# Kernel tuning notes

Measured on AMD Instinct MI355X. Metric: run time of the kernel, lower is better.

Reference implementation:

```python
import jax, jax.numpy as jnp
import numpy as np

B, L, F_DIM, H = 4, 384, 640, 128
K_COULOMB = 332.0
DIELECTRIC = 80.0
BN_EPS = 1e-5

# amino-acid charge table, index order 'ACDEFGHIKLMNPQRSTVWY'
_AA = 'ACDEFGHIKLMNPQRSTVWY'
_CHG = {'D': -1.0, 'E': -1.0, 'K': 1.0, 'R': 1.0, 'H': 0.1}
_TABLE = np.zeros((20, 3), dtype=np.float32)
for _i, _aa in enumerate(_AA):
    c = _CHG.get(_aa, 0.0)
    _TABLE[_i, 0 if c > 0 else (1 if c < 0 else 2)] = 1.0
CHG_TABLE = jnp.asarray(_TABLE)


def _conv1d(x, w, b, pad):
    # x: [N, Cin, L], w: [Cout, Cin, K]
    y = jax.lax.conv_general_dilated(x, w, (1,), [(pad, pad)],
                                     dimension_numbers=('NCH', 'OIH', 'NCH'))
    return y + b[None, :, None]


def setup_inputs() -> dict:
    key = jax.random.key(0)
    ks = jax.random.split(key, 32)
    s = 0.05

    def rn(k, shape):
        return (jax.random.normal(k, shape) * s).astype(jnp.float32)

    inp = {
        'features': jax.random.normal(ks[0], (B, L, F_DIM), dtype=jnp.float32),
        'seq_ids': jax.random.randint(ks[1], (B, L), 0, 20, dtype=jnp.int32),
        'structures': (jax.random.normal(ks[2], (B, L, 3)) * 10.0).astype(jnp.float32),
        # charge predictor: Linear(F,H) -> ReLU -> BN(H) -> Linear(H,H//2) -> ReLU -> Linear(H//2,3) -> Softmax
        'W1': rn(ks[3], (F_DIM, H)), 'b1': jnp.zeros((H,), jnp.float32),
        'gamma': jnp.ones((H,), jnp.float32), 'beta': jnp.zeros((H,), jnp.float32),
        'rmean': jnp.zeros((H,), jnp.float32), 'rvar': jnp.ones((H,), jnp.float32),
        'W2': rn(ks[4], (H, H // 2)), 'b2': jnp.zeros((H // 2,), jnp.float32),
        'W3': rn(ks[5], (H // 2, 3)), 'b3': jnp.zeros((3,), jnp.float32),
        # salt bridge detector: Linear(2F+1,H) -> ReLU -> Linear(H,64) -> ReLU -> Linear(64,1) -> Sigmoid
        'sW1': rn(ks[6], (2 * F_DIM + 1, H)), 'sb1': jnp.zeros((H,), jnp.float32),
        'sW2': rn(ks[7], (H, 64)), 'sb2': jnp.zeros((64,), jnp.float32),
        'sW3': rn(ks[8], (64, 1)), 'sb3': jnp.zeros((1,), jnp.float32),
        # potential calculator convs (OIH layout)
        'c1w': rn(ks[9], (16, 1, 5)), 'c1b': jnp.zeros((16,), jnp.float32),
        'c2w': rn(ks[10], (8, 16, 3)), 'c2b': jnp.zeros((8,), jnp.float32),
        'c3w': rn(ks[11], (1, 8, 3)), 'c3b': jnp.zeros((1,), jnp.float32),
    }
    return inp


def reference(features, seq_ids, structures,
              W1, b1, gamma, beta, rmean, rvar, W2, b2, W3, b3,
              sW1, sb1, sW2, sb2, sW3, sb3,
              c1w, c1b, c2w, c2b, c3w, c3b):
    b_, l_, f_ = features.shape

    # true charges from sequence (one-hot pos/neg/neutral)
    true_charges = CHG_TABLE[seq_ids]                               # [B,L,3]

    # --- charge predictor (BatchNorm in eval mode: running stats) ---
    x = features.reshape(-1, f_)
    h = jax.nn.relu(x @ W1 + b1)
    h = gamma * (h - rmean) / jnp.sqrt(rvar + BN_EPS) + beta
    h = jax.nn.relu(h @ W2 + b2)
    pc = jax.nn.softmax(h @ W3 + b3, axis=-1).reshape(b_, l_, 3)    # [B,L,3]

    net_charge = pc[:, :, 0:1] - pc[:, :, 1:2]                      # [B,L,1]

    # --- electrostatic potential: 1D conv stack on [B,1,L] ---
    p = net_charge.transpose(0, 2, 1)                               # [B,1,L]
    p = jax.nn.relu(_conv1d(p, c1w, c1b, 2))
    p = jax.nn.relu(_conv1d(p, c2w, c2b, 1))
    p = _conv1d(p, c3w, c3b, 1)
    potential = p.transpose(0, 2, 1)                                # [B,L,1]

    # --- pairwise distances ---
    diff = structures[:, :, None, :] - structures[:, None, :, :]    # [B,L,L,3]
    D = jnp.sqrt(jnp.sum(diff * diff, axis=-1) + 1e-12)             # [B,L,L]

    # --- salt bridges: vectorized edge-MLP over all (pos i, neg j) pairs ---
    pos = pc[:, :, 0] > pc[:, :, 2]                                 # [B,L]
    neg = pc[:, :, 1] > pc[:, :, 2]                                 # [B,L]
    a, bb, d = sW1[:f_], sW1[f_:2 * f_], sW1[2 * f_]                # split cat([fi,fj,dist]) @ sW1
    fi = features @ a                                               # [B,L,H]
    fj = features @ bb                                              # [B,L,H]
    hid = jax.nn.relu(fi[:, :, None, :] + fj[:, None, :, :] + D[..., None] * d + sb1)  # [B,L,L,H]
    hid2 = jax.nn.relu(hid @ sW2 + sb2)                             # [B,L,L,64]
    prob = jax.nn.sigmoid((hid2 @ sW3 + sb3)[..., 0])               # [B,L,L]
    q = pos[:, :, None] & neg[:, None, :] & (D < 4.0) & (prob > 0.5)
    salt_bridge_masks = (q | q.transpose(0, 2, 1)).astype(jnp.float32)  # [B,L,L]

    # --- Coulomb energy with distance-dependent dielectric ---
    # dielectric = eps * D / 4 -> e_ij = k * q_i q_j / (eps/4 * D^2)
    qc = pc[:, :, 0] - pc[:, :, 1]                                  # [B,L]
    valid = (D < 15.0) & (D > 0.0)
    triu = jnp.triu(jnp.ones((l_, l_), bool), k=1)[None]
    D_safe = jnp.where(valid, D, 1.0)
    e_ij = K_COULOMB * qc[:, :, None] * qc[:, None, :] / ((DIELECTRIC / 4.0) * D_safe * D_safe)
    energy = jnp.sum(jnp.where(valid & triu, e_ij, 0.0), axis=(1, 2))  # [B]

    return (pc, true_charges, net_charge, potential, salt_bridge_masks, energy)
```

## Files before the change

kernel.cpp:

```cpp
#include <hip/hip_runtime.h>

#define LSEQ 384
#define NROWS 1536
#define FDIM 640
#define HDIM 128
#define PART 196608

#define WS_H1P 0
#define WS_FIP (4*PART)
#define WS_FJP (8*PART)
#define WS_FI  (12*PART)
#define WS_FJ  (13*PART)
#define WS_QC  (14*PART)
#define WS_FLAG (WS_QC + NROWS)

#define OUT_PC    0
#define OUT_TC    4608
#define OUT_NET   9216
#define OUT_POT   10752
#define OUT_MASK  12288
#define OUT_EN    602112

typedef float f4 __attribute__((ext_vector_type(4)));

__device__ __forceinline__ void gl16(const float* g, float* l) {
    __builtin_amdgcn_global_load_lds((const __attribute__((address_space(1))) float*)g,
                                     (__attribute__((address_space(3))) float*)l, 16, 0, 0);
}

__global__ __launch_bounds__(256) void k_gemm(const float* __restrict__ X,
                                              const float* __restrict__ W1,
                                              const float* __restrict__ sW1,
                                              float* __restrict__ ws,
                                              float* __restrict__ out) {
    __shared__ __align__(16) float As[2][32][36];
    __shared__ __align__(16) float Bs[2][32][128];

    const int t = threadIdx.x;
    if (blockIdx.x == 0 && blockIdx.y == 0 && t < 4)
        out[OUT_EN + t] = 0.0f;

    const int m0 = blockIdx.x * 32;
    const int by = blockIdx.y;
    const int mat = by >> 2, kz = by & 3;
    const float* W = (mat == 0) ? W1 : (mat == 1 ? sW1 : sW1 + FDIM * HDIM);
    float* O = ws + (mat == 0 ? WS_H1P : (mat == 1 ? WS_FIP : WS_FJP)) + kz * PART;
    const int k0 = kz * 160;

    const int lane = t & 63, wv = t >> 6;
    const int rg = t >> 5;
    const int cg = t & 31;
    const int ar = t >> 3, ac4 = (t & 7) * 4;

    auto stage_B = [&](int buf, int kk) {
        const float* src = W + (long)kk * HDIM;
        float* dst = &Bs[buf][0][0];
#pragma unroll
        for (int i = 0; i < 4; i++) {
            const int c = wv * 4 + i;
            gl16(src + c * 256 + lane * 4, dst + c * 256);
        }
    };

    f4 acc[4];
    acc[0] = acc[1] = acc[2] = acc[3] = (f4){0.f, 0.f, 0.f, 0.f};

    stage_B(0, k0);
    {
        f4 av = *(const f4*)&X[(long)(m0 + ar) * FDIM + k0 + ac4];
        As[0][ac4 + 0][ar] = av[0];
        As[0][ac4 + 1][ar] = av[1];
        As[0][ac4 + 2][ar] = av[2];
        As[0][ac4 + 3][ar] = av[3];
    }
    __syncthreads();

    for (int kt = 0; kt < 5; kt++) {
        const int buf = kt & 1;
        f4 av;
        if (kt < 4) {
            const int kk = k0 + (kt + 1) * 32;
            stage_B(buf ^ 1, kk);
            av = *(const f4*)&X[(long)(m0 + ar) * FDIM + kk + ac4];
        }
        const float* Ab = &As[buf][0][0];
        const float* Bb = &Bs[buf][0][0];
#pragma unroll
        for (int k = 0; k < 32; k++) {
            f4 a = *(const f4*)&Ab[k * 36 + rg * 4];
            f4 b = *(const f4*)&Bb[k * 128 + cg * 4];
            acc[0] += a[0] * b;
            acc[1] += a[1] * b;
            acc[2] += a[2] * b;
            acc[3] += a[3] * b;
        }
        if (kt < 4) {
            As[(buf ^ 1)][ac4 + 0][ar] = av[0];
            As[(buf ^ 1)][ac4 + 1][ar] = av[1];
            As[(buf ^ 1)][ac4 + 2][ar] = av[2];
            As[(buf ^ 1)][ac4 + 3][ar] = av[3];
        }
        __syncthreads();
    }

#pragma unroll
    for (int r = 0; r < 4; r++)
        *(f4*)&O[(long)(m0 + rg * 4 + r) * HDIM + cg * 4] = acc[r];
}

__global__ __launch_bounds__(256) void k_row(float* __restrict__ ws,
                                             const float* __restrict__ b1,
                                             const float* __restrict__ gam,
                                             const float* __restrict__ bet,
                                             const float* __restrict__ rmean,
                                             const float* __restrict__ rvar,
                                             const float* __restrict__ W2,
                                             const float* __restrict__ b2,
                                             const float* __restrict__ W3,
                                             const float* __restrict__ b3,
                                             const int* __restrict__ seq,
                                             float* __restrict__ out) {
    const int t = threadIdx.x, w = t >> 6, lane = t & 63;
    const int row = blockIdx.x * 4 + w;
    const long base = (long)row * 128;
    const float* h1p = ws + WS_H1P;
    const float* fip = ws + WS_FIP;
    const float* fjp = ws + WS_FJP;

    {
        float fi0 = fip[base + lane] + fip[PART + base + lane]
                  + fip[2 * PART + base + lane] + fip[3 * PART + base + lane];
        float fi1 = fip[base + 64 + lane] + fip[PART + base + 64 + lane]
                  + fip[2 * PART + base + 64 + lane] + fip[3 * PART + base + 64 + lane];
        float fj0 = fjp[base + lane] + fjp[PART + base + lane]
                  + fjp[2 * PART + base + lane] + fjp[3 * PART + base + lane];
        float fj1 = fjp[base + 64 + lane] + fjp[PART + base + 64 + lane]
                  + fjp[2 * PART + base + 64 + lane] + fjp[3 * PART + base + 64 + lane];
        ws[WS_FI + base + lane]      = fi0;
        ws[WS_FI + base + 64 + lane] = fi1;
        ws[WS_FJ + base + lane]      = fj0;
        ws[WS_FJ + base + 64 + lane] = fj1;
    }

    float h0 = h1p[base + lane] + h1p[PART + base + lane]
             + h1p[2 * PART + base + lane] + h1p[3 * PART + base + lane];
    float h1 = h1p[base + 64 + lane] + h1p[PART + base + 64 + lane]
             + h1p[2 * PART + base + 64 + lane] + h1p[3 * PART + base + 64 + lane];
    h0 = fmaxf(h0 + b1[lane], 0.0f);
    h1 = fmaxf(h1 + b1[64 + lane], 0.0f);
    h0 = gam[lane]      * (h0 - rmean[lane])      / sqrtf(rvar[lane] + 1e-5f)      + bet[lane];
    h1 = gam[64 + lane] * (h1 - rmean[64 + lane]) / sqrtf(rvar[64 + lane] + 1e-5f) + bet[64 + lane];

    float acc = b2[lane];
#pragma unroll
    for (int cc = 0; cc < 64; cc++) {
        float wv0 = W2[cc * 64 + lane];
        float wv1 = W2[(cc + 64) * 64 + lane];
        float hv0 = __uint_as_float(__builtin_amdgcn_readlane(__float_as_uint(h0), cc));
        float hv1 = __uint_as_float(__builtin_amdgcn_readlane(__float_as_uint(h1), cc));
        acc = fmaf(hv0, wv0, acc);
        acc = fmaf(hv1, wv1, acc);
    }
    float h2 = fmaxf(acc, 0.0f);
    float x0 = h2 * W3[lane * 3 + 0];
    float x1 = h2 * W3[lane * 3 + 1];
    float x2 = h2 * W3[lane * 3 + 2];
#pragma unroll
    for (int o = 32; o > 0; o >>= 1) {
        x0 += __shfl_xor(x0, o, 64);
        x1 += __shfl_xor(x1, o, 64);
        x2 += __shfl_xor(x2, o, 64);
    }
    if (lane == 0) {
        float l0 = x0 + b3[0], l1 = x1 + b3[1], l2 = x2 + b3[2];
        float m = fmaxf(l0, fmaxf(l1, l2));
        float e0 = expf(l0 - m), e1 = expf(l1 - m), e2 = expf(l2 - m);
        float s = e0 + e1 + e2;
        float pc0 = e0 / s, pc1 = e1 / s, pc2 = e2 / s;
        out[OUT_PC + row * 3 + 0] = pc0;
        out[OUT_PC + row * 3 + 1] = pc1;
        out[OUT_PC + row * 3 + 2] = pc2;
        float net = pc0 - pc1;
        out[OUT_NET + row] = net;
        ws[WS_QC + row] = net;
        ((int*)(ws + WS_FLAG))[row] = (pc0 > pc2 ? 1 : 0) | (pc1 > pc2 ? 2 : 0);
        int sid = seq[row];
        float c0 = (sid == 6 || sid == 8 || sid == 14) ? 1.0f : 0.0f;
        float c1 = (sid == 2 || sid == 3) ? 1.0f : 0.0f;
        out[OUT_TC + row * 3 + 0] = c0;
        out[OUT_TC + row * 3 + 1] = c1;
        out[OUT_TC + row * 3 + 2] = (c0 == 0.0f && c1 == 0.0f) ? 1.0f : 0.0f;
    }
}

__device__ __forceinline__ float mlp_eval(const float* __restrict__ fi, const float* __restrict__ fj,
                                          int gi, int gj, float D,
                                          float dv0, float dv1, float sb0, float sb1v,
                                          float b2v, float w3l, const float* w2s, int lane) {
    float fi0 = fi[(long)gi * 128 + lane];
    float fi1 = fi[(long)gi * 128 + 64 + lane];
    float fj0 = fj[(long)gj * 128 + lane];
    float fj1 = fj[(long)gj * 128 + 64 + lane];
    float h0 = fmaxf(fi0 + fj0 + D * dv0 + sb0, 0.0f);
    float h1 = fmaxf(fi1 + fj1 + D * dv1 + sb1v, 0.0f);
    float a0 = 0.0f, a1 = 0.0f;
#pragma unroll
    for (int cc = 0; cc < 64; cc++) {
        float hv0 = __uint_as_float(__builtin_amdgcn_readlane(__float_as_uint(h0), cc));
        float hv1 = __uint_as_float(__builtin_amdgcn_readlane(__float_as_uint(h1), cc));
        a0 = fmaf(hv0, w2s[cc * 64 + lane], a0);
        a1 = fmaf(hv1, w2s[(cc + 64) * 64 + lane], a1);
    }
    float x = fmaxf(a0 + a1 + b2v, 0.0f) * w3l;
#pragma unroll
    for (int o = 32; o > 0; o >>= 1) x += __shfl_xor(x, o, 64);
    return x;
}

__global__ __launch_bounds__(256) void k2(const float* __restrict__ S,
                                          const float* __restrict__ ws,
                                          const float* __restrict__ sW1,
                                          const float* __restrict__ sb1,
                                          const float* __restrict__ sW2,
                                          const float* __restrict__ sb2,
                                          const float* __restrict__ sW3,
                                          const float* __restrict__ sb3,
                                          const float* __restrict__ c1w, const float* __restrict__ c1b,
                                          const float* __restrict__ c2w, const float* __restrict__ c2b,
                                          const float* __restrict__ c3w, const float* __restrict__ c3b,
                                          float* __restrict__ out) {
    __shared__ char smem[40960];
    const int t = threadIdx.x;
    const int bi = blockIdx.x;

    if (bi < 4) {
        float* p0 = (float*)smem;
        float* p1 = p0 + 388;
        float* p2 = p1 + 16 * 386;
        const int b = bi;
        for (int j = t; j < LSEQ; j += 256) p0[j + 2] = out[OUT_NET + b * LSEQ + j];
        if (t < 2) { p0[t] = 0.0f; p0[LSEQ + 2 + t] = 0.0f; }
        if (t < 16) { p1[t * 386] = 0.0f; p1[t * 386 + 385] = 0.0f; }
        if (t < 8)  { p2[t * 386] = 0.0f; p2[t * 386 + 385] = 0.0f; }
        __syncthreads();
        for (int pos = t; pos < LSEQ; pos += 256) {
#pragma unroll
            for (int o = 0; o < 16; o++) {
                float acc = c1b[o];
#pragma unroll
                for (int k = 0; k < 5; k++) acc = fmaf(p0[pos + k], c1w[o * 5 + k], acc);
                p1[o * 386 + pos + 1] = fmaxf(acc, 0.0f);
            }
        }
        __syncthreads();
        for (int pos = t; pos < LSEQ; pos += 256) {
#pragma unroll
            for (int o = 0; o < 8; o++) {
                float acc = c2b[o];
                for (int i = 0; i < 16; i++)
#pragma unroll
                    for (int k = 0; k < 3; k++)
                        acc = fmaf(p1[i * 386 + pos + k], c2w[(o * 16 + i) * 3 + k], acc);
                p2[o * 386 + pos + 1] = fmaxf(acc, 0.0f);
            }
        }
        __syncthreads();
        for (int pos = t; pos < LSEQ; pos += 256) {
            float acc = c3b[0];
            for (int i = 0; i < 8; i++)
#pragma unroll
                for (int k = 0; k < 3; k++)
                    acc = fmaf(p2[i * 386 + pos + k], c3w[i * 3 + k], acc);
            out[OUT_POT + b * LSEQ + pos] = acc;
        }
        return;
    }

    float* sx = (float*)smem;
    float* sy = sx + 384;
    float* sz = sy + 384;
    float* sq = sz + 384;
    unsigned int* clist = (unsigned int*)(sz + 768);
    unsigned char* sf = (unsigned char*)(smem + 7680);
    float* red = (float*)(smem + 8064);
    int* cntL = (int*)(smem + 8080);
    float* w2s = (float*)(smem + 8192);

    const float* qc = ws + WS_QC;
    const int* flags = (const int*)(ws + WS_FLAG);
    const float* fi = ws + WS_FI;
    const float* fj = ws + WS_FJ;

    const int row = bi - 4;
    const int b = row / LSEQ;
    const int i = row - b * LSEQ;

    for (int j = t; j < LSEQ; j += 256) {
        int g = b * LSEQ + j;
        sx[j] = S[g * 3 + 0];
        sy[j] = S[g * 3 + 1];
        sz[j] = S[g * 3 + 2];
        sq[j] = qc[g];
        sf[j] = (unsigned char)flags[g];
    }
    if (t == 0) *cntL = 0;
    __syncthreads();

    const float six = sx[i], siy = sy[i], siz = sz[i], qi = sq[i];
    const int fli = sf[i];
    const bool posi = (fli & 1) != 0, negi = (fli & 2) != 0;
    const int lane = t & 63, w = t >> 6;
    float esum = 0.0f;
    float* mrow = out + OUT_MASK + (long)row * LSEQ;

    for (int j = t; j < LSEQ; j += 256) {
        float dx = __fsub_rn(six, sx[j]);
        float dy = __fsub_rn(siy, sy[j]);
        float dz = __fsub_rn(siz, sz[j]);
        float d2 = __fadd_rn(__fadd_rn(__fmul_rn(dx, dx), __fmul_rn(dy, dy)), __fmul_rn(dz, dz));
        d2 = __fadd_rn(d2, 1e-12f);
        float D = __fsqrt_rn(d2);
        mrow[j] = 0.0f;
        if (j > i && D < 15.0f && D > 0.0f) {
            float num = __fmul_rn(__fmul_rn(332.0f, qi), sq[j]);
            float den = __fmul_rn(__fmul_rn(20.0f, D), D);
            esum += __fdiv_rn(num, den);
        }
        int flj = sf[j];
        bool near = (D < 4.0f);
        bool need1 = near && posi && ((flj & 2) != 0);
        bool need2 = near && negi && ((flj & 1) != 0);
        if (need1 || need2) {
            int p = atomicAdd(cntL, 1);
            clist[p] = (unsigned int)j | (need1 ? 512u : 0u) | (need2 ? 1024u : 0u);
        }
    }
#pragma unroll
    for (int o = 32; o > 0; o >>= 1) esum += __shfl_xor(esum, o, 64);
    if (lane == 0) red[w] = esum;
    __syncthreads();
    if (t == 0) {
        float s = red[0] + red[1] + red[2] + red[3];
        atomicAdd(&out[OUT_EN + b], s);
    }

    int nc = *cntL;
    if (nc == 0) return;

    for (int idx = t; idx < 2048; idx += 256)
        ((float4*)w2s)[idx] = ((const float4*)sW2)[idx];
    const float* dvec = sW1 + 1280 * 128;
    const float dv0 = dvec[lane], dv1 = dvec[lane + 64];
    const float sb0 = sb1[lane], sb1v = sb1[lane + 64];
    const float w3l = sW3[lane];
    const float b2v = sb2[lane];
    const float b3v = sb3[0];
    __syncthreads();

    for (int c = w; c < nc; c += 4) {
        unsigned int e = clist[c];
        int j = (int)(e & 511u);
        bool need1 = (e & 512u) != 0, need2 = (e & 1024u) != 0;
        float dx = __fsub_rn(six, sx[j]);
        float dy = __fsub_rn(siy, sy[j]);
        float dz = __fsub_rn(siz, sz[j]);
        float d2 = __fadd_rn(__fadd_rn(__fmul_rn(dx, dx), __fmul_rn(dy, dy)), __fmul_rn(dz, dz));
        d2 = __fadd_rn(d2, 1e-12f);
        float D = __fsqrt_rn(d2);
        int gi = row, gj = b * LSEQ + j;
        bool hit = false;
        if (need1) {
            float x = mlp_eval(fi, fj, gi, gj, D, dv0, dv1, sb0, sb1v, b2v, w3l, w2s, lane);
            hit = (x + b3v) > 0.0f;
        }
        if (!hit && need2) {
            float x = mlp_eval(fi, fj, gj, gi, D, dv0, dv1, sb0, sb1v, b2v, w3l, w2s, lane);
            hit = (x + b3v) > 0.0f;
        }
        if (hit && lane == 0) mrow[j] = 1.0f;
    }
}

extern "C" void kernel_launch(void* const* d_in, const int* in_sizes, int n_in,
                              void* d_out, int out_size, void* d_ws, size_t ws_size,
                              hipStream_t stream) {
    const float* X     = (const float*)d_in[0];
    const int*   seq   = (const int*)d_in[1];
    const float* S     = (const float*)d_in[2];
    const float* W1    = (const float*)d_in[3];
    const float* b1    = (const float*)d_in[4];
    const float* gam   = (const float*)d_in[5];
    const float* bet   = (const float*)d_in[6];
    const float* rmean = (const float*)d_in[7];
    const float* rvar  = (const float*)d_in[8];
    const float* W2    = (const float*)d_in[9];
    const float* b2    = (const float*)d_in[10];
    const float* W3    = (const float*)d_in[11];
    const float* b3    = (const float*)d_in[12];
    const float* sW1   = (const float*)d_in[13];
    const float* sb1   = (const float*)d_in[14];
    const float* sW2   = (const float*)d_in[15];
    const float* sb2   = (const float*)d_in[16];
    const float* sW3   = (const float*)d_in[17];
    const float* sb3   = (const float*)d_in[18];
    const float* c1w   = (const float*)d_in[19];
    const float* c1b   = (const float*)d_in[20];
    const float* c2w   = (const float*)d_in[21];
    const float* c2b   = (const float*)d_in[22];
    const float* c3w   = (const float*)d_in[23];
    const float* c3b   = (const float*)d_in[24];

    float* out = (float*)d_out;
    float* ws  = (float*)d_ws;

    hipLaunchKernelGGL(k_gemm, dim3(48, 12), dim3(256), 0, stream, X, W1, sW1, ws, out);
    hipLaunchKernelGGL(k_row, dim3(384), dim3(256), 0, stream,
                       ws, b1, gam, bet, rmean, rvar, W2, b2, W3, b3, seq, out);
    hipLaunchKernelGGL(k2, dim3(1540), dim3(256), 0, stream,
                       S, ws, sW1, sb1, sW2, sb2, sW3, sb3,
                       c1w, c1b, c2w, c2b, c3w, c3b, out);
}
```

Before: 161.2 us.

## Fuse split-K reduction and row MLP into GEMM tail; batch k2 rows per block

Removes the separate k_row kernel. The last-arriving split-K block for each 32-row tile, found with an atomic counter, reduces the partials and runs the charge MLP for 8 rows per wave, reusing W2 loads across those rows. The pairwise kernel now processes 4 rows per block instead of 1, cutting the grid from 1540 to 388 blocks and loading sW2 into LDS at most once per block. The cost is an extra memset, threadfence and atomic overhead, a serial tail on a few blocks, and fewer k2 blocks, which may reduce parallelism.

```diff
diff --git a/kernel.cpp b/kernel.cpp
--- a/kernel.cpp
+++ b/kernel.cpp
@@ -13,6 +13,7 @@
 #define WS_FJ  (13*PART)
 #define WS_QC  (14*PART)
 #define WS_FLAG (WS_QC + NROWS)
+#define WS_CTR  (WS_FLAG + NROWS)
 
 #define OUT_PC    0
 #define OUT_TC    4608
@@ -31,10 +32,21 @@
 __global__ __launch_bounds__(256) void k_gemm(const float* __restrict__ X,
                                               const float* __restrict__ W1,
                                               const float* __restrict__ sW1,
+                                              const float* __restrict__ b1,
+                                              const float* __restrict__ gam,
+                                              const float* __restrict__ bet,
+                                              const float* __restrict__ rmean,
+                                              const float* __restrict__ rvar,
+                                              const float* __restrict__ W2,
+                                              const float* __restrict__ b2,
+                                              const float* __restrict__ W3,
+                                              const float* __restrict__ b3,
+                                              const int* __restrict__ seq,
                                               float* __restrict__ ws,
                                               float* __restrict__ out) {
     __shared__ __align__(16) float As[2][32][36];
     __shared__ __align__(16) float Bs[2][32][128];
+    __shared__ int s_old;
 
     const int t = threadIdx.x;
     if (blockIdx.x == 0 && blockIdx.y == 0 && t < 4)
@@ -106,90 +118,97 @@
 #pragma unroll
     for (int r = 0; r < 4; r++)
         *(f4*)&O[(long)(m0 + rg * 4 + r) * HDIM + cg * 4] = acc[r];
-}
-
-__global__ __launch_bounds__(256) void k_row(float* __restrict__ ws,
-                                             const float* __restrict__ b1,
-                                             const float* __restrict__ gam,
-                                             const float* __restrict__ bet,
-                                             const float* __restrict__ rmean,
-                                             const float* __restrict__ rvar,
-                                             const float* __restrict__ W2,
-                                             const float* __restrict__ b2,
-                                             const float* __restrict__ W3,
-                                             const float* __restrict__ b3,
-                                             const int* __restrict__ seq,
-                                             float* __restrict__ out) {
-    const int t = threadIdx.x, w = t >> 6, lane = t & 63;
-    const int row = blockIdx.x * 4 + w;
-    const long base = (long)row * 128;
+
+    __threadfence();
+    if (t == 0) {
+        int* ctr = (int*)(ws + WS_CTR);
+        s_old = atomicAdd(&ctr[mat * 48 + blockIdx.x], 1);
+    }
+    __syncthreads();
+    if (s_old != 3) return;
+    __threadfence();
+
+    if (mat != 0) {
+        const float* P = ws + (mat == 1 ? WS_FIP : WS_FJP);
+        float* F = ws + (mat == 1 ? WS_FI : WS_FJ);
+        const long base = (long)m0 * 128;
+        for (int e = t; e < 1024; e += 256) {
+            const long off = base + (long)e * 4;
+            f4 v0 = *(const f4*)&P[off];
+            f4 v1 = *(const f4*)&P[PART + off];
+            f4 v2 = *(const f4*)&P[2 * PART + off];
+            f4 v3 = *(const f4*)&P[3 * PART + off];
+            f4 s = ((v0 + v1) + v2) + v3;
+            *(f4*)&F[off] = s;
+        }
+        return;
+    }
+
     const float* h1p = ws + WS_H1P;
-    const float* fip = ws + WS_FIP;
-    const float* fjp = ws + WS_FJP;
-
-    {
-        float fi0 = fip[base + lane] + fip[PART + base + lane]
-                  + fip[2 * PART + base + lane] + fip[3 * PART + base + lane];
-        float fi1 = fip[base + 64 + lane] + fip[PART + base + 64 + lane]
-                  + fip[2 * PART + base + 64 + lane] + fip[3 * PART + base + 64 + lane];
-        float fj0 = fjp[base + lane] + fjp[PART + base + lane]
-                  + fjp[2 * PART + base + lane] + fjp[3 * PART + base + lane];
-        float fj1 = fjp[base + 64 + lane] + fjp[PART + base + 64 + lane]
-                  + fjp[2 * PART + base + 64 + lane] + fjp[3 * PART + base + 64 + lane];
-        ws[WS_FI + base + lane]      = fi0;
-        ws[WS_FI + base + 64 + lane] = fi1;
-        ws[WS_FJ + base + lane]      = fj0;
-        ws[WS_FJ + base + 64 + lane] = fj1;
-    }
-
-    float h0 = h1p[base + lane] + h1p[PART + base + lane]
-             + h1p[2 * PART + base + lane] + h1p[3 * PART + base + lane];
-    float h1 = h1p[base + 64 + lane] + h1p[PART + base + 64 + lane]
-             + h1p[2 * PART + base + 64 + lane] + h1p[3 * PART + base + 64 + lane];
-    h0 = fmaxf(h0 + b1[lane], 0.0f);
-    h1 = fmaxf(h1 + b1[64 + lane], 0.0f);
-    h0 = gam[lane]      * (h0 - rmean[lane])      / sqrtf(rvar[lane] + 1e-5f)      + bet[lane];
-    h1 = gam[64 + lane] * (h1 - rmean[64 + lane]) / sqrtf(rvar[64 + lane] + 1e-5f) + bet[64 + lane];
-
-    float acc = b2[lane];
-#pragma unroll
+    float h0[8], h1[8];
+#pragma unroll
+    for (int rr = 0; rr < 8; rr++) {
+        const int row = m0 + wv * 8 + rr;
+        const long base = (long)row * 128;
+        float a0 = h1p[base + lane] + h1p[PART + base + lane]
+                 + h1p[2 * PART + base + lane] + h1p[3 * PART + base + lane];
+        float a1 = h1p[base + 64 + lane] + h1p[PART + base + 64 + lane]
+                 + h1p[2 * PART + base + 64 + lane] + h1p[3 * PART + base + 64 + lane];
+        a0 = fmaxf(a0 + b1[lane], 0.0f);
+        a1 = fmaxf(a1 + b1[64 + lane], 0.0f);
+        h0[rr] = gam[lane]      * (a0 - rmean[lane])      / sqrtf(rvar[lane] + 1e-5f)      + bet[lane];
+        h1[rr] = gam[64 + lane] * (a1 - rmean[64 + lane]) / sqrtf(rvar[64 + lane] + 1e-5f) + bet[64 + lane];
+    }
+
+    const float b2v = b2[lane];
+    float a2[8];
+#pragma unroll
+    for (int rr = 0; rr < 8; rr++) a2[rr] = b2v;
+#pragma unroll 4
     for (int cc = 0; cc < 64; cc++) {
-        float wv0 = W2[cc * 64 + lane];
-        float wv1 = W2[(cc + 64) * 64 + lane];
-        float hv0 = __uint_as_float(__builtin_amdgcn_readlane(__float_as_uint(h0), cc));
-        float hv1 = __uint_as_float(__builtin_amdgcn_readlane(__float_as_uint(h1), cc));
-        acc = fmaf(hv0, wv0, acc);
-        acc = fmaf(hv1, wv1, acc);
-    }
-    float h2 = fmaxf(acc, 0.0f);
-    float x0 = h2 * W3[lane * 3 + 0];
-    float x1 = h2 * W3[lane * 3 + 1];
-    float x2 = h2 * W3[lane * 3 + 2];
-#pragma unroll
-    for (int o = 32; o > 0; o >>= 1) {
-        x0 += __shfl_xor(x0, o, 64);
-        x1 += __shfl_xor(x1, o, 64);
-        x2 += __shfl_xor(x2, o, 64);
-    }
-    if (lane == 0) {
-        float l0 = x0 + b3[0], l1 = x1 + b3[1], l2 = x2 + b3[2];
-        float m = fmaxf(l0, fmaxf(l1, l2));
-        float e0 = expf(l0 - m), e1 = expf(l1 - m), e2 = expf(l2 - m);
-        float s = e0 + e1 + e2;
-        float pc0 = e0 / s, pc1 = e1 / s, pc2 = e2 / s;
-        out[OUT_PC + row * 3 + 0] = pc0;
-        out[OUT_PC + row * 3 + 1] = pc1;
-        out[OUT_PC + row * 3 + 2] = pc2;
-        float net = pc0 - pc1;
-        out[OUT_NET + row] = net;
-        ws[WS_QC + row] = net;
-        ((int*)(ws + WS_FLAG))[row] = (pc0 > pc2 ? 1 : 0) | (pc1 > pc2 ? 2 : 0);
-        int sid = seq[row];
-        float c0 = (sid == 6 || sid == 8 || sid == 14) ? 1.0f : 0.0f;
-        float c1 = (sid == 2 || sid == 3) ? 1.0f : 0.0f;
-        out[OUT_TC + row * 3 + 0] = c0;
-        out[OUT_TC + row * 3 + 1] = c1;
-        out[OUT_TC + row * 3 + 2] = (c0 == 0.0f && c1 == 0.0f) ? 1.0f : 0.0f;
+        const float wv0 = W2[cc * 64 + lane];
+        const float wv1 = W2[(cc + 64) * 64 + lane];
+#pragma unroll
+        for (int rr = 0; rr < 8; rr++) {
+            float hv0 = __uint_as_float(__builtin_amdgcn_readlane(__float_as_uint(h0[rr]), cc));
+            float hv1 = __uint_as_float(__builtin_amdgcn_readlane(__float_as_uint(h1[rr]), cc));
+            a2[rr] = fmaf(hv0, wv0, a2[rr]);
+            a2[rr] = fmaf(hv1, wv1, a2[rr]);
+        }
+    }
+
+    const float w30 = W3[lane * 3 + 0], w31 = W3[lane * 3 + 1], w32 = W3[lane * 3 + 2];
+#pragma unroll
+    for (int rr = 0; rr < 8; rr++) {
+        float h2 = fmaxf(a2[rr], 0.0f);
+        float x0 = h2 * w30, x1 = h2 * w31, x2 = h2 * w32;
+#pragma unroll
+        for (int o = 32; o > 0; o >>= 1) {
+            x0 += __shfl_xor(x0, o, 64);
+            x1 += __shfl_xor(x1, o, 64);
+            x2 += __shfl_xor(x2, o, 64);
+        }
+        if (lane == 0) {
+            const int row = m0 + wv * 8 + rr;
+            float l0 = x0 + b3[0], l1 = x1 + b3[1], l2 = x2 + b3[2];
+            float m = fmaxf(l0, fmaxf(l1, l2));
+            float e0 = expf(l0 - m), e1 = expf(l1 - m), e2 = expf(l2 - m);
+            float s = e0 + e1 + e2;
+            float pc0 = e0 / s, pc1 = e1 / s, pc2 = e2 / s;
+            out[OUT_PC + row * 3 + 0] = pc0;
+            out[OUT_PC + row * 3 + 1] = pc1;
+            out[OUT_PC + row * 3 + 2] = pc2;
+            float net = pc0 - pc1;
+            out[OUT_NET + row] = net;
+            ws[WS_QC + row] = net;
+            ((int*)(ws + WS_FLAG))[row] = (pc0 > pc2 ? 1 : 0) | (pc1 > pc2 ? 2 : 0);
+            int sid = seq[row];
+            float c0 = (sid == 6 || sid == 8 || sid == 14) ? 1.0f : 0.0f;
+            float c1 = (sid == 2 || sid == 3) ? 1.0f : 0.0f;
+            out[OUT_TC + row * 3 + 0] = c0;
+            out[OUT_TC + row * 3 + 1] = c1;
+            out[OUT_TC + row * 3 + 2] = (c0 == 0.0f && c1 == 0.0f) ? 1.0f : 0.0f;
+        }
     }
 }
 
@@ -280,10 +299,11 @@
     float* sy = sx + 384;
     float* sz = sy + 384;
     float* sq = sz + 384;
-    unsigned int* clist = (unsigned int*)(sz + 768);
+    unsigned int* clist = (unsigned int*)(sx + 1536);
     unsigned char* sf = (unsigned char*)(smem + 7680);
     float* red = (float*)(smem + 8064);
     int* cntL = (int*)(smem + 8080);
+    int* w2flag = (int*)(smem + 8084);
     float* w2s = (float*)(smem + 8192);
 
     const float* qc = ws + WS_QC;
@@ -291,9 +311,9 @@
     const float* fi = ws + WS_FI;
     const float* fj = ws + WS_FJ;
 
-    const int row = bi - 4;
-    const int b = row / LSEQ;
-    const int i = row - b * LSEQ;
+    const int rowblk = bi - 4;
+    const int b = rowblk / 96;
+    const int i0 = (rowblk % 96) * 4;
 
     for (int j = t; j < LSEQ; j += 256) {
         int g = b * LSEQ + j;
@@ -303,38 +323,88 @@
         sq[j] = qc[g];
         sf[j] = (unsigned char)flags[g];
     }
-    if (t == 0) *cntL = 0;
+    if (t == 0) *w2flag = 0;
     __syncthreads();
 
-    const float six = sx[i], siy = sy[i], siz = sz[i], qi = sq[i];
-    const int fli = sf[i];
-    const bool posi = (fli & 1) != 0, negi = (fli & 2) != 0;
     const int lane = t & 63, w = t >> 6;
+    const float* dvec = sW1 + 1280 * 128;
+    const float dv0 = dvec[lane], dv1 = dvec[lane + 64];
+    const float sb0 = sb1[lane], sb1v = sb1[lane + 64];
+    const float w3l = sW3[lane];
+    const float b2v = sb2[lane];
+    const float b3v = sb3[0];
+
     float esum = 0.0f;
-    float* mrow = out + OUT_MASK + (long)row * LSEQ;
-
-    for (int j = t; j < LSEQ; j += 256) {
-        float dx = __fsub_rn(six, sx[j]);
-        float dy = __fsub_rn(siy, sy[j]);
-        float dz = __fsub_rn(siz, sz[j]);
-        float d2 = __fadd_rn(__fadd_rn(__fmul_rn(dx, dx), __fmul_rn(dy, dy)), __fmul_rn(dz, dz));
-        d2 = __fadd_rn(d2, 1e-12f);
-        float D = __fsqrt_rn(d2);
-        mrow[j] = 0.0f;
-        if (j > i && D < 15.0f && D > 0.0f) {
-            float num = __fmul_rn(__fmul_rn(332.0f, qi), sq[j]);
-            float den = __fmul_rn(__fmul_rn(20.0f, D), D);
-            esum += __fdiv_rn(num, den);
-        }
-        int flj = sf[j];
-        bool near = (D < 4.0f);
-        bool need1 = near && posi && ((flj & 2) != 0);
-        bool need2 = near && negi && ((flj & 1) != 0);
-        if (need1 || need2) {
-            int p = atomicAdd(cntL, 1);
-            clist[p] = (unsigned int)j | (need1 ? 512u : 0u) | (need2 ? 1024u : 0u);
-        }
-    }
+
+    for (int r = 0; r < 4; r++) {
+        const int i = i0 + r;
+        const int grow = b * LSEQ + i;
+        if (t == 0) *cntL = 0;
+        __syncthreads();
+
+        const float six = sx[i], siy = sy[i], siz = sz[i], qi = sq[i];
+        const int fli = sf[i];
+        const bool posi = (fli & 1) != 0, negi = (fli & 2) != 0;
+        float* mrow = out + OUT_MASK + (long)grow * LSEQ;
+
+        for (int j = t; j < LSEQ; j += 256) {
+            float dx = __fsub_rn(six, sx[j]);
+            float dy = __fsub_rn(siy, sy[j]);
+            float dz = __fsub_rn(siz, sz[j]);
+            float d2 = __fadd_rn(__fadd_rn(__fmul_rn(dx, dx), __fmul_rn(dy, dy)), __fmul_rn(dz, dz));
+            d2 = __fadd_rn(d2, 1e-12f);
+            float D = __fsqrt_rn(d2);
+            mrow[j] = 0.0f;
+            if (j > i && D < 15.0f && D > 0.0f) {
+                float num = __fmul_rn(__fmul_rn(332.0f, qi), sq[j]);
+                float den = __fmul_rn(__fmul_rn(20.0f, D), D);
+                esum += __fdiv_rn(num, den);
+            }
+            int flj = sf[j];
+            bool near = (D < 4.0f);
+            bool need1 = near && posi && ((flj & 2) != 0);
+            bool need2 = near && negi && ((flj & 1) != 0);
+            if (need1 || need2) {
+                int p = atomicAdd(cntL, 1);
+                clist[p] = (unsigned int)j | (need1 ? 512u : 0u) | (need2 ? 1024u : 0u);
+            }
+        }
+        __syncthreads();
+
+        int nc = *cntL;
+        if (nc > 0) {
+            if (!*w2flag) {
+                for (int idx = t; idx < 2048; idx += 256)
+                    ((float4*)w2s)[idx] = ((const float4*)sW2)[idx];
+                __syncthreads();
+                if (t == 0) *w2flag = 1;
+            }
+            for (int c = w; c < nc; c += 4) {
+                unsigned int e = clist[c];
+                int j = (int)(e & 511u);
+                bool need1 = (e & 512u) != 0, need2 = (e & 1024u) != 0;
+                float dx = __fsub_rn(six, sx[j]);
+                float dy = __fsub_rn(siy, sy[j]);
+                float dz = __fsub_rn(siz, sz[j]);
+                float d2 = __fadd_rn(__fadd_rn(__fmul_rn(dx, dx), __fmul_rn(dy, dy)), __fmul_rn(dz, dz));
+                d2 = __fadd_rn(d2, 1e-12f);
+                float D = __fsqrt_rn(d2);
+                int gi = grow, gj = b * LSEQ + j;
+                bool hit = false;
+                if (need1) {
+                    float x = mlp_eval(fi, fj, gi, gj, D, dv0, dv1, sb0, sb1v, b2v, w3l, w2s, lane);
+                    hit = (x + b3v) > 0.0f;
+                }
+                if (!hit && need2) {
+                    float x = mlp_eval(fi, fj, gj, gi, D, dv0, dv1, sb0, sb1v, b2v, w3l, w2s, lane);
+                    hit = (x + b3v) > 0.0f;
+                }
+                if (hit && lane == 0) mrow[j] = 1.0f;
+            }
+        }
+        __syncthreads();
+    }
+
 #pragma unroll
     for (int o = 32; o > 0; o >>= 1) esum += __shfl_xor(esum, o, 64);
     if (lane == 0) red[w] = esum;
@@ -342,42 +412,6 @@
     if (t == 0) {
         float s = red[0] + red[1] + red[2] + red[3];
         atomicAdd(&out[OUT_EN + b], s);
-    }
-
-    int nc = *cntL;
-    if (nc == 0) return;
-
-    for (int idx = t; idx < 2048; idx += 256)
-        ((float4*)w2s)[idx] = ((const float4*)sW2)[idx];
-    const float* dvec = sW1 + 1280 * 128;
-    const float dv0 = dvec[lane], dv1 = dvec[lane + 64];
-    const float sb0 = sb1[lane], sb1v = sb1[lane + 64];
-    const float w3l = sW3[lane];
-    const float b2v = sb2[lane];
-    const float b3v = sb3[0];
-    __syncthreads();
-
-    for (int c = w; c < nc; c += 4) {
-        unsigned int e = clist[c];
-        int j = (int)(e & 511u);
-        bool need1 = (e & 512u) != 0, need2 = (e & 1024u) != 0;
-        float dx = __fsub_rn(six, sx[j]);
-        float dy = __fsub_rn(siy, sy[j]);
-        float dz = __fsub_rn(siz, sz[j]);
-        float d2 = __fadd_rn(__fadd_rn(__fmul_rn(dx, dx), __fmul_rn(dy, dy)), __fmul_rn(dz, dz));
-        d2 = __fadd_rn(d2, 1e-12f);
-        float D = __fsqrt_rn(d2);
-        int gi = row, gj = b * LSEQ + j;
-        bool hit = false;
-        if (need1) {
-            float x = mlp_eval(fi, fj, gi, gj, D, dv0, dv1, sb0, sb1v, b2v, w3l, w2s, lane);
-            hit = (x + b3v) > 0.0f;
-        }
-        if (!hit && need2) {
-            float x = mlp_eval(fi, fj, gj, gi, D, dv0, dv1, sb0, sb1v, b2v, w3l, w2s, lane);
-            hit = (x + b3v) > 0.0f;
-        }
-        if (hit && lane == 0) mrow[j] = 1.0f;
     }
 }
 
@@ -413,10 +447,11 @@
     float* out = (float*)d_out;
     float* ws  = (float*)d_ws;
 
-    hipLaunchKernelGGL(k_gemm, dim3(48, 12), dim3(256), 0, stream, X, W1, sW1, ws, out);
-    hipLaunchKernelGGL(k_row, dim3(384), dim3(256), 0, stream,
-                       ws, b1, gam, bet, rmean, rvar, W2, b2, W3, b3, seq, out);
-    hipLaunchKernelGGL(k2, dim3(1540), dim3(256), 0, stream,
+    hipMemsetAsync(ws + WS_CTR, 0, 144 * sizeof(int), stream);
+
+    hipLaunchKernelGGL(k_gemm, dim3(48, 12), dim3(256), 0, stream,
+                       X, W1, sW1, b1, gam, bet, rmean, rvar, W2, b2, W3, b3, seq, ws, out);
+    hipLaunchKernelGGL(k2, dim3(388), dim3(256), 0, stream,
                        S, ws, sW1, sb1, sW2, sb2, sW3, sb3,
                        c1w, c1b, c2w, c2b, c3w, c3b, out);
 }
```

Result: slower. 229.4 us (+42.3%).
